# Performance work log

Hardware: AMD Instinct MI355X
Metric: run time of the kernel (lower is better)

## Reference

```python
import jax, jax.numpy as jnp
import numpy as np

# hardcoded constants from Model.sample_regions / gather_regions / __init__
RADIUS = 0.4
REGIONS = 50
BALL_K = 1000
TOP_K = 4
NEIGHBORHOOD = 128
COURSE = 512


def square_distance(src, dst):
    """src [B,N,C], dst [B,M,C] -> squared dists [B,N,M]."""
    d = -2.0 * jnp.einsum('bnc,bmc->bnm', src, dst)
    d = d + jnp.sum(src * src, -1)[:, :, None]
    d = d + jnp.sum(dst * dst, -1)[:, None, :]
    return d


def furthest_point_sample(xyz, npoint):
    """xyz [B,N,3] -> indices [B,npoint] (deterministic start at point 0)."""
    B, N, _ = xyz.shape
    barange = jnp.arange(B)

    def body(carry, _):
        dist, last = carry                      # dist [B,N], last [B] int32
        centroid = xyz[barange, last]           # [B,3]
        d = jnp.sum((xyz - centroid[:, None, :]) ** 2, -1)
        dist = jnp.minimum(dist, d)
        nxt = jnp.argmax(dist, axis=-1).astype(jnp.int32)
        return (dist, nxt), last

    init = (jnp.full((B, N), 1e10, xyz.dtype), jnp.zeros((B,), jnp.int32))
    _, idxs = jax.lax.scan(body, init, None, length=npoint)
    return jnp.transpose(idxs)                  # [B, npoint]


def knn_point(k, xyz, new_xyz):
    """k-NN of new_xyz [B,S,3] among xyz [B,N,3] -> idx [B,S,k]."""
    d = square_distance(new_xyz, xyz)
    _, idx = jax.lax.top_k(-d, k)
    return idx


def gather_xyz(xyz, idx):
    """xyz [B,N,3], idx [B,S] -> [B,S,3]."""
    B = xyz.shape[0]
    return xyz[jnp.arange(B)[:, None], idx]


def gather_regions(p_xyz, a_xyz, radius):
    """p_xyz [B,N,3] points, a_xyz [B,A,3] anchors -> [B, TOP_K*NEIGHBORHOOD, 3]."""
    B = p_xyz.shape[0]
    d2 = square_distance(a_xyz, p_xyz)                       # [B,A,N]
    counts = jnp.minimum(jnp.sum(d2 < radius * radius, axis=2), BALL_K)
    _, topk_idx = jax.lax.top_k(counts, TOP_K)               # densest anchors [B,TOP_K]
    sel = gather_xyz(a_xyz, topk_idx)                        # [B,TOP_K,3]
    nidx = knn_point(NEIGHBORHOOD, p_xyz, sel)               # [B,TOP_K,NB]
    neigh = p_xyz[jnp.arange(B)[:, None, None], nidx]        # [B,TOP_K,NB,3]
    return neigh.reshape(B, TOP_K * NEIGHBORHOOD, 3)


def sample_regions(p_xyz, regions, r):
    anchors_idx = furthest_point_sample(p_xyz, regions)
    anchors = gather_xyz(p_xyz, anchors_idx)
    return gather_regions(p_xyz, anchors, r)


def setup_inputs() -> dict:
    key = jax.random.key(0)
    points = jax.random.normal(key, (16, 3, 16384), dtype=jnp.float32)
    return {"points": points}


def reference(points):
    # points [B,3,N] -> p_xyz [B,N,3]
    p_xyz = jnp.transpose(points, (0, 2, 1))
    roi1 = sample_regions(p_xyz, REGIONS, RADIUS)            # [B,512,3]
    roi2 = sample_regions(p_xyz, REGIONS, RADIUS)            # [B,512,3] (a == b == 0.4)
    fps_idx = furthest_point_sample(p_xyz, COURSE)           # [B,512]
    fps_pts = gather_xyz(p_xyz, fps_idx)                     # [B,512,3]
    return jnp.concatenate([roi1, roi2, fps_pts], axis=1)    # [B,1536,3]
```

## Files before the change

### kernel.cpp

```cpp
#include <hip/hip_runtime.h>
#include <stdint.h>

#define NPTS 16384
#define BATCH 16
#define FPS_N 512
#define NANCH 50
#define TOPK 4
#define NBH 128
#define BALLK 1000

#define FT 1024
#define FPPT (NPTS / FT)

#define CTRL_XOR1 0xB1
#define CTRL_XOR2 0x4E
#define CTRL_ROR4 0x124
#define CTRL_ROR8 0x128

#define DPP_MAX64(v, CTRL) do {                                                   \
  unsigned int _lo = (unsigned int)(v);                                           \
  unsigned int _hi = (unsigned int)((v) >> 32);                                   \
  unsigned int _slo = (unsigned int)__builtin_amdgcn_update_dpp((int)_lo, (int)_lo, CTRL, 0xf, 0xf, false); \
  unsigned int _shi = (unsigned int)__builtin_amdgcn_update_dpp((int)_hi, (int)_hi, CTRL, 0xf, 0xf, false); \
  unsigned long long _o = (((unsigned long long)_shi) << 32) | _slo;              \
  if (_o > (v)) (v) = _o;                                                         \
} while (0)

#define DPP_MIN64(v, CTRL) do {                                                   \
  unsigned int _lo = (unsigned int)(v);                                           \
  unsigned int _hi = (unsigned int)((v) >> 32);                                   \
  unsigned int _slo = (unsigned int)__builtin_amdgcn_update_dpp((int)_lo, (int)_lo, CTRL, 0xf, 0xf, false); \
  unsigned int _shi = (unsigned int)__builtin_amdgcn_update_dpp((int)_hi, (int)_hi, CTRL, 0xf, 0xf, false); \
  unsigned long long _o = (((unsigned long long)_shi) << 32) | _slo;              \
  if (_o < (v)) (v) = _o;                                                         \
} while (0)

#define SWZ16_MAX64(v) do {                                                       \
  unsigned int _lo = (unsigned int)(v), _hi = (unsigned int)((v) >> 32);          \
  unsigned int _slo = (unsigned int)__builtin_amdgcn_ds_swizzle((int)_lo, 0x401f);\
  unsigned int _shi = (unsigned int)__builtin_amdgcn_ds_swizzle((int)_hi, 0x401f);\
  unsigned long long _o = (((unsigned long long)_shi) << 32) | _slo;              \
  if (_o > (v)) (v) = _o;                                                         \
} while (0)

#define SWZ16_MIN64(v) do {                                                       \
  unsigned int _lo = (unsigned int)(v), _hi = (unsigned int)((v) >> 32);          \
  unsigned int _slo = (unsigned int)__builtin_amdgcn_ds_swizzle((int)_lo, 0x401f);\
  unsigned int _shi = (unsigned int)__builtin_amdgcn_ds_swizzle((int)_hi, 0x401f);\
  unsigned long long _o = (((unsigned long long)_shi) << 32) | _slo;              \
  if (_o < (v)) (v) = _o;                                                         \
} while (0)

#define SHF32_MAX64(v) do {                                                       \
  unsigned long long _o = __shfl_xor((v), 32, 64);                                \
  if (_o > (v)) (v) = _o;                                                         \
} while (0)

#define SHF32_MIN64(v) do {                                                       \
  unsigned long long _o = __shfl_xor((v), 32, 64);                                \
  if (_o < (v)) (v) = _o;                                                         \
} while (0)

__global__ __launch_bounds__(FT) void fps_kernel(const float* __restrict__ pts,
                                                 int* __restrict__ fps_idx) {
  const int b = blockIdx.x;
  const int tid = threadIdx.x;
  const float* __restrict__ px = pts + (size_t)b * 3 * NPTS;
  const float* __restrict__ py = px + NPTS;
  const float* __restrict__ pz = py + NPTS;

  float x[FPPT], y[FPPT], z[FPPT], dist[FPPT];
#pragma unroll
  for (int k = 0; k < FPPT; ++k) {
    const int i = tid + k * FT;
    x[k] = px[i]; y[k] = py[i]; z[k] = pz[i];
    dist[k] = 1e10f;
  }
  __shared__ unsigned long long waveres[2][16];
  if (tid == 0) fps_idx[b * FPS_N] = 0;
  float bx = px[0], by = py[0], bz = pz[0];

  for (int step = 1; step < FPS_N; ++step) {
    float bd = -1.0f;
    int bk = 0;
#pragma unroll
    for (int k = 0; k < FPPT; ++k) {
      const float dx = __fsub_rn(x[k], bx);
      const float dy = __fsub_rn(y[k], by);
      const float dz = __fsub_rn(z[k], bz);
      const float d = __fadd_rn(__fadd_rn(__fmul_rn(dx, dx), __fmul_rn(dy, dy)),
                                __fmul_rn(dz, dz));
      const float dk = fminf(dist[k], d);
      dist[k] = dk;
      if (dk > bd) { bd = dk; bk = k; }
    }
    const uint32_t bi = (uint32_t)tid + ((uint32_t)bk << 10);
    unsigned long long key =
        ((unsigned long long)__float_as_uint(bd) << 32) | (uint32_t)(~bi);

    DPP_MAX64(key, CTRL_XOR1);
    DPP_MAX64(key, CTRL_XOR2);
    DPP_MAX64(key, CTRL_ROR4);
    DPP_MAX64(key, CTRL_ROR8);
    SWZ16_MAX64(key);
    SHF32_MAX64(key);

    const int par = step & 1;
    if ((tid & 63) == 0) waveres[par][tid >> 6] = key;
    __syncthreads();

    unsigned long long g = waveres[par][tid & 15];
    DPP_MAX64(g, CTRL_XOR1);
    DPP_MAX64(g, CTRL_XOR2);
    DPP_MAX64(g, CTRL_ROR4);
    DPP_MAX64(g, CTRL_ROR8);

    const uint32_t widx = ~(uint32_t)g;
    if (tid == 0) fps_idx[b * FPS_N + step] = (int)widx;
    bx = px[widx]; by = py[widx]; bz = pz[widx];
  }
}

__global__ __launch_bounds__(256) void count_kernel(const float* __restrict__ pts,
                                                    const int* __restrict__ fps_idx,
                                                    int* __restrict__ counts) {
  const int b = blockIdx.y, a = blockIdx.x;
  const int tid = threadIdx.x;
  const float* __restrict__ px = pts + (size_t)b * 3 * NPTS;
  const float* __restrict__ py = px + NPTS;
  const float* __restrict__ pz = py + NPTS;
  const int aidx = fps_idx[b * FPS_N + a];
  const float ax = px[aidx], ay = py[aidx], az = pz[aidx];
  const float asum = __fadd_rn(__fadd_rn(__fmul_rn(ax, ax), __fmul_rn(ay, ay)),
                               __fmul_rn(az, az));
  const float R2 = (float)(0.4 * 0.4);
  int cnt = 0;
  for (int i = tid; i < NPTS; i += 256) {
    const float X = px[i], Y = py[i], Z = pz[i];
    const float dot = __fadd_rn(__fadd_rn(__fmul_rn(ax, X), __fmul_rn(ay, Y)),
                                __fmul_rn(az, Z));
    const float psum = __fadd_rn(__fadd_rn(__fmul_rn(X, X), __fmul_rn(Y, Y)),
                                 __fmul_rn(Z, Z));
    const float d = __fadd_rn(__fadd_rn(__fmul_rn(-2.0f, dot), asum), psum);
    cnt += (d < R2) ? 1 : 0;
  }
#pragma unroll
  for (int off = 32; off > 0; off >>= 1) cnt += __shfl_xor(cnt, off, 64);
  __shared__ int ws[4];
  if ((tid & 63) == 0) ws[tid >> 6] = cnt;
  __syncthreads();
  if (tid == 0) {
    int c = ws[0] + ws[1] + ws[2] + ws[3];
    counts[b * NANCH + a] = c < BALLK ? c : BALLK;
  }
}

__global__ void top4_kernel(const int* __restrict__ counts,
                            const int* __restrict__ fps_idx,
                            int* __restrict__ top4pt) {
  const int b = threadIdx.x;
  if (b >= BATCH) return;
  unsigned long long used = 0ULL;
  for (int r = 0; r < TOPK; ++r) {
    int bestc = -1, besta = 0;
    for (int a = 0; a < NANCH; ++a) {
      if (used & (1ULL << a)) continue;
      const int c = counts[b * NANCH + a];
      if (c > bestc) { bestc = c; besta = a; }
    }
    used |= 1ULL << besta;
    top4pt[b * TOPK + r] = fps_idx[b * FPS_N + besta];
  }
}

#define KT 1024
#define KPPT (NPTS / KT)

__device__ __forceinline__ uint32_t f2key(float f) {
  uint32_t u = __float_as_uint(f);
  return (u & 0x80000000u) ? ~u : (u | 0x80000000u);
}

__global__ __launch_bounds__(KT) void knn_kernel(const float* __restrict__ pts,
                                                 const int* __restrict__ top4pt,
                                                 int* __restrict__ nn_idx) {
  const int b = blockIdx.y, j = blockIdx.x;
  const int tid = threadIdx.x;
  const float* __restrict__ px = pts + (size_t)b * 3 * NPTS;
  const float* __restrict__ py = px + NPTS;
  const float* __restrict__ pz = py + NPTS;
  const int aidx = top4pt[b * TOPK + j];
  const float ax = px[aidx], ay = py[aidx], az = pz[aidx];
  const float asum = __fadd_rn(__fadd_rn(__fmul_rn(ax, ax), __fmul_rn(ay, ay)),
                               __fmul_rn(az, az));
  unsigned long long key[KPPT];
#pragma unroll
  for (int k = 0; k < KPPT; ++k) {
    const int i = tid + k * KT;
    const float X = px[i], Y = py[i], Z = pz[i];
    const float dot = __fadd_rn(__fadd_rn(__fmul_rn(ax, X), __fmul_rn(ay, Y)),
                                __fmul_rn(az, Z));
    const float psum = __fadd_rn(__fadd_rn(__fmul_rn(X, X), __fmul_rn(Y, Y)),
                                 __fmul_rn(Z, Z));
    const float d = __fadd_rn(__fadd_rn(__fmul_rn(-2.0f, dot), asum), psum);
    key[k] = ((unsigned long long)f2key(d) << 32) | (uint32_t)i;
  }
  __shared__ unsigned long long waveres[2][16];
  for (int t = 0; t < NBH; ++t) {
    unsigned long long m01 = key[0] < key[1] ? key[0] : key[1];
    unsigned long long m23 = key[2] < key[3] ? key[2] : key[3];
    unsigned long long m45 = key[4] < key[5] ? key[4] : key[5];
    unsigned long long m67 = key[6] < key[7] ? key[6] : key[7];
    unsigned long long m89 = key[8] < key[9] ? key[8] : key[9];
    unsigned long long mab = key[10] < key[11] ? key[10] : key[11];
    unsigned long long mcd = key[12] < key[13] ? key[12] : key[13];
    unsigned long long mef = key[14] < key[15] ? key[14] : key[15];
    unsigned long long m0 = m01 < m23 ? m01 : m23;
    unsigned long long m1 = m45 < m67 ? m45 : m67;
    unsigned long long m2 = m89 < mab ? m89 : mab;
    unsigned long long m3 = mcd < mef ? mcd : mef;
    unsigned long long ma = m0 < m1 ? m0 : m1;
    unsigned long long mb = m2 < m3 ? m2 : m3;
    unsigned long long m = ma < mb ? ma : mb;

    DPP_MIN64(m, CTRL_XOR1);
    DPP_MIN64(m, CTRL_XOR2);
    DPP_MIN64(m, CTRL_ROR4);
    DPP_MIN64(m, CTRL_ROR8);
    SWZ16_MIN64(m);
    SHF32_MIN64(m);

    const int par = t & 1;
    if ((tid & 63) == 0) waveres[par][tid >> 6] = m;
    __syncthreads();
    unsigned long long g = waveres[par][tid & 15];
    DPP_MIN64(g, CTRL_XOR1);
    DPP_MIN64(g, CTRL_XOR2);
    DPP_MIN64(g, CTRL_ROR4);
    DPP_MIN64(g, CTRL_ROR8);

    if (tid == 0) nn_idx[(b * TOPK + j) * NBH + t] = (int)(uint32_t)g;
#pragma unroll
    for (int k = 0; k < KPPT; ++k)
      if (key[k] == g) key[k] = ~0ULL;
  }
}

__global__ __launch_bounds__(512) void gather_kernel(const float* __restrict__ pts,
                                                     const int* __restrict__ nn_idx,
                                                     const int* __restrict__ fps_idx,
                                                     float* __restrict__ out) {
  const int b = blockIdx.x, t = threadIdx.x;
  const float* __restrict__ px = pts + (size_t)b * 3 * NPTS;
  const float* __restrict__ py = px + NPTS;
  const float* __restrict__ pz = py + NPTS;
  for (int s = t; s < 1536; s += 512) {
    int src;
    if (s < 1024) src = nn_idx[b * 512 + (s & 511)];
    else          src = fps_idx[b * FPS_N + (s - 1024)];
    float* o = out + ((size_t)b * 1536 + s) * 3;
    o[0] = px[src]; o[1] = py[src]; o[2] = pz[src];
  }
}

extern "C" void kernel_launch(void* const* d_in, const int* in_sizes, int n_in,
                              void* d_out, int out_size, void* d_ws, size_t ws_size,
                              hipStream_t stream) {
  const float* pts = (const float*)d_in[0];
  float* out = (float*)d_out;
  char* ws = (char*)d_ws;
  int* fps_idx = (int*)(ws);
  int* counts  = (int*)(ws + 32768);
  int* top4pt  = (int*)(ws + 40960);
  int* nn_idx  = (int*)(ws + 49152);

  fps_kernel<<<dim3(BATCH), dim3(FT), 0, stream>>>(pts, fps_idx);
  count_kernel<<<dim3(NANCH, BATCH), dim3(256), 0, stream>>>(pts, fps_idx, counts);
  top4_kernel<<<dim3(1), dim3(64), 0, stream>>>(counts, fps_idx, top4pt);
  knn_kernel<<<dim3(TOPK, BATCH), dim3(KT), 0, stream>>>(pts, top4pt, nn_idx);
  gather_kernel<<<dim3(BATCH), dim3(512), 0, stream>>>(pts, nn_idx, fps_idx, out);
}
```

Measured before the change: 1.056 ms.

## Rework FPS inner loop with packed-f32 math, LDS-resident coords, ballot argmax

The FPS kernel now keeps x and y in LDS as float2 pairs and only z and the running distances in registers. Distances are computed with packed v_pk_add/mul_f32 inline assembly. The per-step argmax is split: a 32-bit max-value wave reduction first, then ballots to find the lowest matching index, which replaces the 64-bit key shuffles. This is meant to cut VALU work and reduction latency on the serial 511-step critical path. The cost is LDS reads every step and a 128KB+ dynamic shared-memory allocation per block. Tie-breaking must still pick the lowest index, which the ballot/ctz logic tries to preserve.

```diff
diff --git a/kernel.cpp b/kernel.cpp
--- a/kernel.cpp
+++ b/kernel.cpp
@@ -10,7 +10,9 @@
 #define BALLK 1000
 
 #define FT 1024
-#define FPPT (NPTS / FT)
+#define FPAIRS 8
+
+#define FPS_SMEM (65536 + 65536 + 2 * 16 * 8)
 
 #define CTRL_XOR1 0xB1
 #define CTRL_XOR2 0x4E
@@ -35,14 +37,6 @@
   if (_o < (v)) (v) = _o;                                                         \
 } while (0)
 
-#define SWZ16_MAX64(v) do {                                                       \
-  unsigned int _lo = (unsigned int)(v), _hi = (unsigned int)((v) >> 32);          \
-  unsigned int _slo = (unsigned int)__builtin_amdgcn_ds_swizzle((int)_lo, 0x401f);\
-  unsigned int _shi = (unsigned int)__builtin_amdgcn_ds_swizzle((int)_hi, 0x401f);\
-  unsigned long long _o = (((unsigned long long)_shi) << 32) | _slo;              \
-  if (_o > (v)) (v) = _o;                                                         \
-} while (0)
-
 #define SWZ16_MIN64(v) do {                                                       \
   unsigned int _lo = (unsigned int)(v), _hi = (unsigned int)((v) >> 32);          \
   unsigned int _slo = (unsigned int)__builtin_amdgcn_ds_swizzle((int)_lo, 0x401f);\
@@ -51,73 +45,103 @@
   if (_o < (v)) (v) = _o;                                                         \
 } while (0)
 
-#define SHF32_MAX64(v) do {                                                       \
-  unsigned long long _o = __shfl_xor((v), 32, 64);                                \
-  if (_o > (v)) (v) = _o;                                                         \
-} while (0)
-
 #define SHF32_MIN64(v) do {                                                       \
   unsigned long long _o = __shfl_xor((v), 32, 64);                                \
   if (_o < (v)) (v) = _o;                                                         \
 } while (0)
 
-__global__ __launch_bounds__(FT) void fps_kernel(const float* __restrict__ pts,
-                                                 int* __restrict__ fps_idx) {
+__global__ __launch_bounds__(FT, 4) void fps_kernel(const float* __restrict__ pts,
+                                                    int* __restrict__ fps_idx) {
+  extern __shared__ char smem[];
+  float2* __restrict__ X2 = (float2*)smem;
+  float2* __restrict__ Y2 = (float2*)(smem + 65536);
+  unsigned long long* __restrict__ waveres =
+      (unsigned long long*)(smem + 131072);
+
   const int b = blockIdx.x;
-  const int tid = threadIdx.x;
+  const int t = threadIdx.x;
   const float* __restrict__ px = pts + (size_t)b * 3 * NPTS;
   const float* __restrict__ py = px + NPTS;
   const float* __restrict__ pz = py + NPTS;
 
-  float x[FPPT], y[FPPT], z[FPPT], dist[FPPT];
-#pragma unroll
-  for (int k = 0; k < FPPT; ++k) {
-    const int i = tid + k * FT;
-    x[k] = px[i]; y[k] = py[i]; z[k] = pz[i];
-    dist[k] = 1e10f;
-  }
-  __shared__ unsigned long long waveres[2][16];
-  if (tid == 0) fps_idx[b * FPS_N] = 0;
+  float2 z2[FPAIRS], dist2[FPAIRS];
+#pragma unroll
+  for (int j = 0; j < FPAIRS; ++j) {
+    const int i2 = (j << 11) + (t << 1);
+    X2[(j << 10) + t] = *(const float2*)&px[i2];
+    Y2[(j << 10) + t] = *(const float2*)&py[i2];
+    z2[j] = *(const float2*)&pz[i2];
+    dist2[j] = make_float2(1e10f, 1e10f);
+  }
+  if (t == 0) fps_idx[b * FPS_N] = 0;
   float bx = px[0], by = py[0], bz = pz[0];
+  const int wS = __builtin_amdgcn_readfirstlane(t >> 6);
+  __syncthreads();
 
   for (int step = 1; step < FPS_N; ++step) {
-    float bd = -1.0f;
-    int bk = 0;
-#pragma unroll
-    for (int k = 0; k < FPPT; ++k) {
-      const float dx = __fsub_rn(x[k], bx);
-      const float dy = __fsub_rn(y[k], by);
-      const float dz = __fsub_rn(z[k], bz);
-      const float d = __fadd_rn(__fadd_rn(__fmul_rn(dx, dx), __fmul_rn(dy, dy)),
-                                __fmul_rn(dz, dz));
-      const float dk = fminf(dist[k], d);
-      dist[k] = dk;
-      if (dk > bd) { bd = dk; bk = k; }
+    const float nbx = -bx, nby = -by, nbz = -bz;
+    const float2 nbx2 = make_float2(nbx, nbx);
+    const float2 nby2 = make_float2(nby, nby);
+    const float2 nbz2 = make_float2(nbz, nbz);
+    float run = -1.0f;
+#pragma unroll
+    for (int j = 0; j < FPAIRS; ++j) {
+      const float2 Xp = X2[(j << 10) + t];
+      const float2 Yp = Y2[(j << 10) + t];
+      float2 t0, t1, t2;
+      asm("v_pk_add_f32 %0, %3, %6\n\t"
+          "v_pk_add_f32 %1, %4, %7\n\t"
+          "v_pk_add_f32 %2, %5, %8\n\t"
+          "v_pk_mul_f32 %0, %0, %0\n\t"
+          "v_pk_mul_f32 %1, %1, %1\n\t"
+          "v_pk_mul_f32 %2, %2, %2\n\t"
+          "v_pk_add_f32 %0, %0, %1\n\t"
+          "v_pk_add_f32 %0, %0, %2"
+          : "=&v"(t0), "=&v"(t1), "=&v"(t2)
+          : "v"(Xp), "v"(Yp), "v"(z2[j]), "v"(nbx2), "v"(nby2), "v"(nbz2));
+      dist2[j].x = fminf(dist2[j].x, t0.x);
+      dist2[j].y = fminf(dist2[j].y, t0.y);
+      asm("v_max3_f32 %0, %0, %1, %2"
+          : "+v"(run) : "v"(dist2[j].x), "v"(dist2[j].y));
     }
-    const uint32_t bi = (uint32_t)tid + ((uint32_t)bk << 10);
-    unsigned long long key =
-        ((unsigned long long)__float_as_uint(bd) << 32) | (uint32_t)(~bi);
-
-    DPP_MAX64(key, CTRL_XOR1);
-    DPP_MAX64(key, CTRL_XOR2);
-    DPP_MAX64(key, CTRL_ROR4);
-    DPP_MAX64(key, CTRL_ROR8);
-    SWZ16_MAX64(key);
-    SHF32_MAX64(key);
-
+    uint32_t m = __float_as_uint(run);
+    {
+      uint32_t s;
+      s = (uint32_t)__builtin_amdgcn_update_dpp((int)m, (int)m, CTRL_XOR1, 0xf, 0xf, false); m = m > s ? m : s;
+      s = (uint32_t)__builtin_amdgcn_update_dpp((int)m, (int)m, CTRL_XOR2, 0xf, 0xf, false); m = m > s ? m : s;
+      s = (uint32_t)__builtin_amdgcn_update_dpp((int)m, (int)m, CTRL_ROR4, 0xf, 0xf, false); m = m > s ? m : s;
+      s = (uint32_t)__builtin_amdgcn_update_dpp((int)m, (int)m, CTRL_ROR8, 0xf, 0xf, false); m = m > s ? m : s;
+      s = (uint32_t)__builtin_amdgcn_ds_swizzle((int)m, 0x401f);                              m = m > s ? m : s;
+      s = (uint32_t)__shfl_xor((int)m, 32, 64);                                              m = m > s ? m : s;
+    }
+    const float gmaxf = __uint_as_float(m);
+    uint32_t widx_w = 0xFFFFFFFFu;
+#pragma unroll
+    for (int j = 0; j < FPAIRS; ++j) {
+      const unsigned long long b0 = __ballot(dist2[j].x == gmaxf);
+      const unsigned long long b1 = __ballot(dist2[j].y == gmaxf);
+      const unsigned long long cb = b0 | b1;
+      if (cb) {
+        const int l = (int)__builtin_ctzll(cb);
+        const uint32_t p = ((b0 >> l) & 1ull) ? 0u : 1u;
+        const uint32_t cand = ((uint32_t)j << 11) + ((uint32_t)((wS << 6) | l) << 1) + p;
+        widx_w = widx_w < cand ? widx_w : cand;
+      }
+    }
+    const unsigned long long key =
+        ((unsigned long long)m << 32) | (uint32_t)(~widx_w);
     const int par = step & 1;
-    if ((tid & 63) == 0) waveres[par][tid >> 6] = key;
+    if ((t & 63) == 0) waveres[par * 16 + wS] = key;
     __syncthreads();
-
-    unsigned long long g = waveres[par][tid & 15];
+    unsigned long long g = waveres[par * 16 + (t & 15)];
     DPP_MAX64(g, CTRL_XOR1);
     DPP_MAX64(g, CTRL_XOR2);
     DPP_MAX64(g, CTRL_ROR4);
     DPP_MAX64(g, CTRL_ROR8);
-
     const uint32_t widx = ~(uint32_t)g;
-    if (tid == 0) fps_idx[b * FPS_N + step] = (int)widx;
-    bx = px[widx]; by = py[widx]; bz = pz[widx];
+    if (t == 0) fps_idx[b * FPS_N + step] = (int)widx;
+    const int si = __builtin_amdgcn_readfirstlane((int)widx);
+    bx = px[si]; by = py[si]; bz = pz[si];
   }
 }
 
@@ -274,7 +298,10 @@
   int* top4pt  = (int*)(ws + 40960);
   int* nn_idx  = (int*)(ws + 49152);
 
-  fps_kernel<<<dim3(BATCH), dim3(FT), 0, stream>>>(pts, fps_idx);
+  hipFuncSetAttribute((const void*)fps_kernel,
+                      hipFuncAttributeMaxDynamicSharedMemorySize, FPS_SMEM);
+
+  fps_kernel<<<dim3(BATCH), dim3(FT), FPS_SMEM, stream>>>(pts, fps_idx);
   count_kernel<<<dim3(NANCH, BATCH), dim3(256), 0, stream>>>(pts, fps_idx, counts);
   top4_kernel<<<dim3(1), dim3(64), 0, stream>>>(counts, fps_idx, top4pt);
   knn_kernel<<<dim3(TOPK, BATCH), dim3(KT), 0, stream>>>(pts, top4pt, nn_idx);
```

New measurement: 1.073 ms. About the same (+1.6%).
